# Kernel tuning notes

Measured on AMD Instinct MI355X. Metric: run time of the kernel, lower is better.

Reference implementation:

```python
import jax, jax.numpy as jnp
import numpy as np

NEG = -1e30  # log-space 'zero' (safe substitute for -inf)
EPS = 1e-7   # keras.backend.epsilon(), used by ctc_batch_cost


def _ctc_forward(logp, z, allow2):
    """CTC negative log-likelihood via the forward DP in log space.
    logp:   [B, T, C] log-probabilities
    z:      [B, S] extended label sequence (blanks interleaved), S = 2L+1
    allow2: [B, S] bool, whether the skip transition (s-2 -> s) is legal
    Returns [B, 1] loss (matches keras ctc_batch_cost output shape).
    """
    B, T, C = logp.shape
    S = z.shape[1]
    # Gather per-timestep log-probs of extended labels: [B, T, S] -> [T, B, S]
    b_idx = jnp.arange(B)[:, None, None]
    t_idx = jnp.arange(T)[None, :, None]
    lp_z = jnp.transpose(logp[b_idx, t_idx, z[:, None, :]], (1, 0, 2))

    s_idx = jnp.arange(S)[None, :]
    alpha0 = jnp.where(s_idx < 2, lp_z[0], NEG)  # paths may start at blank or first label

    def step(alpha, lp_t):
        a1 = jnp.concatenate([jnp.full((B, 1), NEG, alpha.dtype), alpha[:, :-1]], axis=1)
        a2 = jnp.concatenate([jnp.full((B, 2), NEG, alpha.dtype), alpha[:, :-2]], axis=1)
        a2 = jnp.where(allow2, a2, NEG)
        m = jnp.maximum(alpha, jnp.maximum(a1, a2))
        lse = m + jnp.log(jnp.exp(alpha - m) + jnp.exp(a1 - m) + jnp.exp(a2 - m))
        return lp_t + lse, None

    alphaT, _ = jax.lax.scan(step, alpha0, lp_z[1:])
    # Paths end at last blank (S-1) or last label (S-2)
    last, last2 = alphaT[:, -1], alphaT[:, -2]
    m = jnp.maximum(last, last2)
    ll = m + jnp.log(jnp.exp(last - m) + jnp.exp(last2 - m))
    return -ll[:, None]


def setup_inputs() -> dict:
    key = jax.random.key(0)
    k1, k2 = jax.random.split(key)
    B, T, C, L = 32, 2048, 256, 256
    # ctc_batch_cost expects post-softmax probabilities
    y_pred = jax.nn.softmax(jax.random.normal(k1, (B, T, C), jnp.float32), axis=-1)
    y_true = jax.random.randint(k2, (B, L), 0, C - 1)  # blank = C-1 excluded from labels
    return {"y_true": y_true, "y_pred": y_pred}


def reference(y_true, y_pred):
    B, T, C = y_pred.shape
    blank = C - 1
    L = y_true.shape[1]
    S = 2 * L + 1
    labels = y_true.astype(jnp.int32)
    # Extended label sequence: blank, l0, blank, l1, ..., blank
    z = jnp.full((B, S), blank, jnp.int32).at[:, 1::2].set(labels)
    z_m2 = jnp.concatenate([jnp.full((B, 2), -1, jnp.int32), z[:, :-2]], axis=1)
    allow2 = (z != blank) & (z != z_m2)
    logp = jnp.log(y_pred + EPS)
    return _ctc_forward(logp, z, allow2)
```

## Files before the change

### kernel.cpp

```cpp
#include <hip/hip_runtime.h>

#define TT   2048
#define CC   256
#define LL   256
#define SS   513
#define TM   1023
#define EPSF (1e-7f)
#define LN2F (0.69314718055994531f)
#define DPTH 8
#define RBTH 64
#define NCH  127
#define EMINI (-2000000000)
#define GSTR 260

#if __has_builtin(__builtin_amdgcn_frexp_expf)
#define FREXP_EXP __builtin_amdgcn_frexp_expf
#else
static __device__ __forceinline__ int FREXP_EXP(float x){ int e; return (frexpf(x,&e), e); }
#endif
#if __has_builtin(__builtin_amdgcn_ldexpf)
#define LDEXP __builtin_amdgcn_ldexpf
#else
#define LDEXP ldexpf
#endif

__launch_bounds__(256, 4)
__global__ void ctc_gather_kernel(const int* __restrict__ y_true,
                                  const float* __restrict__ y_pred,
                                  float* __restrict__ gat)
{
    const int b   = blockIdx.x;
    const int i   = threadIdx.x;
    const int col = y_true[b * LL + i];
    const float* rp = y_pred + (size_t)b * TT * CC;
    float*       gp = gat    + (size_t)b * TT * GSTR;
    const int tch = TT / gridDim.y;
    const int t0  = blockIdx.y * tch;
    #pragma unroll 4
    for (int t = t0; t < t0 + tch; ++t) {
        gp[(size_t)t * GSTR + i] = rp[(size_t)t * CC + col] + EPSF;
        if (i < 4)
            gp[(size_t)t * GSTR + 256 + i] = rp[(size_t)t * CC + (CC - 1)] + EPSF;
    }
}

template<int NSTEP>
__device__ __forceinline__ void fwd_group(float (&f)[9], int &e, bool &mm,
        const float (&kk)[8], int lane,
        float4 o0, float4 o1, float4 o2, float4 o3,
        float4 q0, float4 q1, float4 q2, float4 q3,
        float b0, float b1, float b2, float b3)
{
    float h[8];
    #pragma unroll
    for (int j = 0; j < 8; ++j) h[j] = __shfl_up(f[j], 1);
    int he = __shfl_up(e, 1);
    if (lane == 0) {
        he = e;
        #pragma unroll
        for (int j = 0; j < 8; ++j) h[j] = 0.0f;
    }
    const int E  = mm ? (e > he ? e : he) : he;
    const int dh = he - E, dn = e - E;
    float g[17];
    #pragma unroll
    for (int j = 0; j < 8; ++j) g[j] = LDEXP(h[j], dh);
    #pragma unroll
    for (int j = 0; j < 9; ++j) g[8 + j] = LDEXP(f[j], dn);
    e = E;

#define FSW(Q, O, B, LO) do {                                                 \
        const float pv[8] = {Q.x,Q.y,Q.z,Q.w,O.x,O.y,O.z,O.w};                \
        _Pragma("unroll")                                                     \
        for (int i = 16; i >= (LO); --i) {                                    \
            if (i & 1) g[i] = (g[i] + g[i-1] + g[i-2]*kk[(i-1)>>1])           \
                              * pv[(i-1)>>1];                                 \
            else       g[i] = (g[i] + g[i-1]) * (B);                          \
        }                                                                     \
    } while (0)

    if (NSTEP == 4) {
        FSW(q0,o0,b0,2); FSW(q1,o1,b1,4); FSW(q2,o2,b2,6); FSW(q3,o3,b3,8);
    } else {
        FSW(q0,o0,b0,4); FSW(q1,o1,b1,6); FSW(q2,o2,b2,8);
    }
#undef FSW

    #pragma unroll
    for (int j = 0; j < 9; ++j) f[j] = g[8 + j];
    float mx = f[0];
    #pragma unroll
    for (int j = 1; j < 9; ++j) mx = fmaxf(mx, f[j]);
    const int em = FREXP_EXP(mx);
    #pragma unroll
    for (int j = 0; j < 9; ++j) f[j] = LDEXP(f[j], -em);
    e += em;
    mm = (mx > 0.0f);
}

template<int NSTEP>
__device__ __forceinline__ void bwd_group(float (&f)[9], int &e, bool &mm,
        const float (&kk)[8], int lane,
        float4 o0, float4 o1, float4 o2, float4 o3,
        float4 q0, float4 q1, float4 q2, float4 q3,
        float b0, float b1, float b2, float b3)
{
    float h[8];
    #pragma unroll
    for (int j = 0; j < 8; ++j) h[j] = __shfl_down(f[j + 1], 1);
    int he = __shfl_down(e, 1);
    if (lane == 63) {
        he = e;
        #pragma unroll
        for (int j = 0; j < 8; ++j) h[j] = 0.0f;
    }
    const int E  = mm ? (e > he ? e : he) : he;
    const int dh = he - E, dn = e - E;
    float g[17];
    #pragma unroll
    for (int j = 0; j < 9; ++j) g[j] = LDEXP(f[j], dn);
    #pragma unroll
    for (int j = 0; j < 8; ++j) g[9 + j] = LDEXP(h[j], dh);
    e = E;

#define BSW(O, Q, B, HI) do {                                                 \
        const float pv[8] = {O.x,O.y,O.z,O.w,Q.x,Q.y,Q.z,Q.w};                \
        _Pragma("unroll")                                                     \
        for (int i = 0; i <= (HI); ++i) {                                     \
            if (i & 1) g[i] = (g[i] + g[i+1] + g[i+2]*kk[(i-1)>>1])           \
                              * pv[(i-1)>>1];                                 \
            else       g[i] = (g[i] + g[i+1]) * (B);                          \
        }                                                                     \
    } while (0)

    if (NSTEP == 4) {
        BSW(o0,q0,b0,14); BSW(o1,q1,b1,12); BSW(o2,q2,b2,10); BSW(o3,q3,b3,8);
    } else {
        BSW(o0,q0,b0,12); BSW(o1,q1,b1,10); BSW(o2,q2,b2,8);
    }
#undef BSW

    #pragma unroll
    for (int j = 0; j < 9; ++j) f[j] = g[j];
    float mx = f[0];
    #pragma unroll
    for (int j = 1; j < 9; ++j) mx = fmaxf(mx, f[j]);
    const int em = FREXP_EXP(mx);
    #pragma unroll
    for (int j = 0; j < 9; ++j) f[j] = LDEXP(f[j], -em);
    e += em;
    mm = (mx > 0.0f);
}

__launch_bounds__(128, 1)
__global__ void ctc_grp_kernel(const int* __restrict__ y_true,
                               const float* __restrict__ y_pred,
                               const float* __restrict__ gat,
                               float* __restrict__ out)
{
    __shared__ float cw[SS];
    __shared__ int   ew[64];

    const int tid   = threadIdx.x;
    const int w     = tid >> 6;
    const int lane  = tid & 63;
    const int b     = blockIdx.x;
    const int blank = CC - 1;

    const int*   lab  = y_true + b * LL;
    const float* base = y_pred + (size_t)b * TT * CC;
    const float* gLb  = gat    + (size_t)b * TT * GSTR;

    float kk[8];
    if (w == 0) {
        #pragma unroll
        for (int j = 0; j < 8; ++j) {
            const int li  = 4 * lane - 4 + j;
            const int lic = li < 0 ? 0 : li;
            const int z   = lab[lic];
            const int zm  = (li >= 1) ? lab[li - 1] : -1;
            kk[j] = (li >= 0 && z != zm) ? 1.0f : 0.0f;
        }
    } else {
        #pragma unroll
        for (int j = 0; j < 8; ++j) {
            const int li  = 4 * lane + j;
            const int lic = li > 255 ? 255 : li;
            const int z   = lab[lic];
            kk[j] = (li <= 254 && lab[li + 1] != z) ? 1.0f : 0.0f;
        }
    }

    float f[9];
    #pragma unroll
    for (int j = 0; j < 9; ++j) f[j] = 0.0f;
    int  e = 0;
    bool mm;

    if (w == 0) {
        if (lane == 0) {
            f[0] = base[blank]  + EPSF;
            f[1] = base[lab[0]] + EPSF;
        }
        mm = (lane == 0);
    } else {
        if (lane == 63) {
            const float* rT = base + (size_t)(TT - 1) * CC;
            f[7] = rT[lab[255]] + EPSF;
            f[8] = rT[blank]    + EPSF;
        }
        mm = (lane == 63);
    }

    const int oofs = 4 * lane;
    const int qofs = (w == 0) ? (4 * lane - 4 < 0 ? 0 : 4 * lane - 4)
                              : (4 * lane + 4);
    const int bofs = 256 + (lane & 3);
    const int dstp = (w == 0) ? GSTR : -GSTR;

    float4 s0o[4], s0q[4]; float s0b[4];

#define LOADG(SO, SQ, SB, ROWP) do {                                          \
        const float* _rp = (ROWP);                                            \
        _Pragma("unroll")                                                     \
        for (int k = 0; k < 4; ++k) {                                         \
            SO[k] = *(const float4*)(_rp + oofs);                             \
            SQ[k] = *(const float4*)(_rp + qofs);                             \
            SB[k] = _rp[bofs];                                                \
            _rp += dstp;                                                      \
        } } while (0)

    const float* grow = (w == 0) ? (gLb + (size_t)1 * GSTR)
                                 : (gLb + (size_t)2046 * GSTR);
    LOADG(s0o, s0q, s0b, grow); grow += 4 * dstp;

    for (int c = 0; c < 255; ++c) {
        const float4 a0 = s0o[0], a1 = s0o[1], a2 = s0o[2], a3 = s0o[3];
        const float4 p0 = s0q[0], p1 = s0q[1], p2 = s0q[2], p3 = s0q[3];
        const float  c0 = s0b[0], c1 = s0b[1], c2 = s0b[2], c3 = s0b[3];
        LOADG(s0o, s0q, s0b, grow); grow += 4 * dstp;
        __builtin_amdgcn_sched_barrier(0);
        if (w == 0) fwd_group<4>(f, e, mm, kk, lane,
                        a0,a1,a2,a3, p0,p1,p2,p3, c0,c1,c2,c3);
        else        bwd_group<4>(f, e, mm, kk, lane,
                        a0,a1,a2,a3, p0,p1,p2,p3, c0,c1,c2,c3);
    }
    {
        const float4 a0 = s0o[0], a1 = s0o[1], a2 = s0o[2], a3 = s0o[3];
        const float4 p0 = s0q[0], p1 = s0q[1], p2 = s0q[2], p3 = s0q[3];
        const float  c0 = s0b[0], c1 = s0b[1], c2 = s0b[2], c3 = s0b[3];
        if (w == 0) fwd_group<3>(f, e, mm, kk, lane,
                        a0,a1,a2,a3, p0,p1,p2,p3, c0,c1,c2,c3);
        else        bwd_group<3>(f, e, mm, kk, lane,
                        a0,a1,a2,a3, p0,p1,p2,p3, c0,c1,c2,c3);
    }
#undef LOADG

    if (w == 1) {
        float d1 = __shfl_down(f[1], 1);
        int   de = __shfl_down(e, 1);
        if (lane == 63) { d1 = 0.0f; de = e; }
        int dlt = de - e;
        if (dlt >= RBTH) {
            #pragma unroll
            for (int j = 0; j < 9; ++j) f[j] = LDEXP(f[j], -dlt);
            e = de; dlt = 0;
        }
        const float bf = LDEXP(d1, dlt);
        float cb[9];
        cb[0] = f[0] + f[1];
        cb[1] = f[1] + f[2] + f[3] * kk[0];
        cb[2] = f[2] + f[3];
        cb[3] = f[3] + f[4] + f[5] * kk[1];
        cb[4] = f[4] + f[5];
        cb[5] = f[5] + f[6] + f[7] * kk[2];
        cb[6] = f[6] + f[7];
        cb[7] = f[7] + f[8] + bf   * kk[3];
        cb[8] = f[8] + bf;
        #pragma unroll
        for (int j = 0; j < 8; ++j) cw[8 * lane + j] = cb[j];
        if (lane == 63) cw[512] = cb[8];
        ew[lane] = e;
    }

    __syncthreads();

    if (w == 0) {
        float part = 0.0f;
        #pragma unroll
        for (int j = 0; j < 8; ++j) part += f[j] * cw[8 * lane + j];
        if (lane == 63) part += f[8] * cw[512];
        int   ep = (part > 0.0f) ? (e + ew[lane]) : EMINI;
        float m  = part;
        #pragma unroll
        for (int d = 1; d < 64; d <<= 1) {
            const float mo = __shfl_xor(m, d);
            const int   eo = __shfl_xor(ep, d);
            const int   E  = ep > eo ? ep : eo;
            m  = LDEXP(m, ep - E) + LDEXP(mo, eo - E);
            ep = E;
        }
        if (lane == 0)
            out[b] = -LN2F * ((float)ep + __builtin_amdgcn_logf(m));
    }
}

__launch_bounds__(128, 1)
__global__ void ctc_fb_kernel(const int* __restrict__ y_true,
                              const float* __restrict__ y_pred,
                              float* __restrict__ out)
{
    __shared__ float cw[SS];
    __shared__ int   ew[64];

    const int tid   = threadIdx.x;
    const int w     = tid >> 6;
    const int lane  = tid & 63;
    const int b     = blockIdx.x;
    const int blank = CC - 1;

    const int*   lab  = y_true + b * LL;
    const float* base = y_pred + (size_t)b * TT * CC;

    int   col[4];
    float kup[4], kdn[4];
    #pragma unroll
    for (int i = 0; i < 4; ++i) {
        const int li = 4 * lane + i;
        const int z  = lab[li];
        col[i] = z;
        const int zm = (li >= 1) ? lab[li - 1] : -1;
        kup[i] = (z != zm) ? 1.0f : 0.0f;
        kdn[i] = (li <= 254 && lab[li + 1] != z) ? 1.0f : 0.0f;
    }

    float f[9];
    #pragma unroll
    for (int j = 0; j < 9; ++j) f[j] = 0.0f;
    int  e = 0;
    bool lzero;

    if (w == 0) {
        if (lane == 0) { f[0] = base[blank] + EPSF; f[1] = base[col[0]] + EPSF; }
        lzero = (lane != 0);
    } else {
        if (lane == 63) {
            const float* rT = base + (size_t)(TT - 1) * CC;
            f[7] = rT[col[3]] + EPSF; f[8] = rT[blank] + EPSF;
        }
        lzero = (lane != 63);
    }

    float pfb[DPTH]; float pfl[DPTH][4];
    #pragma unroll
    for (int k = 0; k < DPTH; ++k) {
        const int r = (w == 0) ? (1 + k) : (TT - 2 - k);
        const float* rp = base + (size_t)r * CC;
        pfb[k] = rp[blank];
        #pragma unroll
        for (int i = 0; i < 4; ++i) pfl[k][i] = rp[col[i]];
    }

    auto renorm = [&]() {
        float m = fmaxf(fmaxf(fmaxf(f[0], f[1]), fmaxf(f[2], f[3])),
                        fmaxf(fmaxf(f[4], f[5]), fmaxf(f[6], fmaxf(f[7], f[8]))));
        const int em = FREXP_EXP(m);
        #pragma unroll
        for (int j = 0; j < 9; ++j) f[j] = LDEXP(f[j], -em);
        e += em;
    };
    auto fwd_step = [&](float pb, float p0, float p1, float p2, float p3) {
        float u7 = __shfl_up(f[7], 1);
        int   ue = __shfl_up(e, 1);
        if (lane == 0) { u7 = 0.0f; ue = e; }
        int dlt = ue - e;
        const bool rb = lzero || (dlt >= RBTH);
        if (__ballot(rb)) {
            const int sh = rb ? -dlt : 0;
            #pragma unroll
            for (int j = 0; j < 9; ++j) f[j] = LDEXP(f[j], sh);
            e = rb ? ue : e; dlt = rb ? 0 : dlt;
            lzero = lzero && (u7 == 0.0f);
        }
        const float bf = LDEXP(u7, dlt);
        const float n0 = (f[0] + bf) * pb;
        const float n1 = (f[1] + f[0] + bf   * kup[0]) * p0;
        const float n2 = (f[2] + f[1]) * pb;
        const float n3 = (f[3] + f[2] + f[1] * kup[1]) * p1;
        const float n4 = (f[4] + f[3]) * pb;
        const float n5 = (f[5] + f[4] + f[3] * kup[2]) * p2;
        const float n6 = (f[6] + f[5]) * pb;
        const float n7 = (f[7] + f[6] + f[5] * kup[3]) * p3;
        const float n8 = (f[8] + f[7]) * pb;
        f[0]=n0; f[1]=n1; f[2]=n2; f[3]=n3; f[4]=n4;
        f[5]=n5; f[6]=n6; f[7]=n7; f[8]=n8;
    };
    auto bwd_step = [&](float pb, float p0, float p1, float p2, float p3) {
        float d1 = __shfl_down(f[1], 1);
        int   de = __shfl_down(e, 1);
        if (lane == 63) { d1 = 0.0f; de = e; }
        int dlt = de - e;
        const bool rb = lzero || (dlt >= RBTH);
        if (__ballot(rb)) {
            const int sh = rb ? -dlt : 0;
            #pragma unroll
            for (int j = 0; j < 9; ++j) f[j] = LDEXP(f[j], sh);
            e = rb ? de : e; dlt = rb ? 0 : dlt;
            lzero = lzero && (d1 == 0.0f);
        }
        const float bf = LDEXP(d1, dlt);
        const float n0 = (f[0] + f[1]) * pb;
        const float n1 = (f[1] + f[2] + f[3] * kdn[0]) * p0;
        const float n2 = (f[2] + f[3]) * pb;
        const float n3 = (f[3] + f[4] + f[5] * kdn[1]) * p1;
        const float n4 = (f[4] + f[5]) * pb;
        const float n5 = (f[5] + f[6] + f[7] * kdn[2]) * p2;
        const float n6 = (f[6] + f[7]) * pb;
        const float n7 = (f[7] + f[8] + bf   * kdn[3]) * p3;
        const float n8 = (f[8] + bf) * pb;
        f[0]=n0; f[1]=n1; f[2]=n2; f[3]=n3; f[4]=n4;
        f[5]=n5; f[6]=n6; f[7]=n7; f[8]=n8;
    };

    if (w == 0) {
        for (int c = 0; c < NCH; ++c) {
            #pragma unroll
            for (int k = 0; k < DPTH; ++k) {
                const float pb = pfb[k] + EPSF;
                const float p0 = pfl[k][0] + EPSF, p1 = pfl[k][1] + EPSF;
                const float p2 = pfl[k][2] + EPSF, p3 = pfl[k][3] + EPSF;
                int tp = 1 + c * DPTH + k + DPTH; if (tp > TM) tp = TM;
                const float* rp = base + (size_t)tp * CC;
                pfb[k] = rp[blank];
                #pragma unroll
                for (int i = 0; i < 4; ++i) pfl[k][i] = rp[col[i]];
                fwd_step(pb, p0, p1, p2, p3);
                if (k == 3 || k == 7) renorm();
            }
        }
        #pragma unroll
        for (int k = 0; k < 7; ++k) {
            fwd_step(pfb[k] + EPSF, pfl[k][0] + EPSF, pfl[k][1] + EPSF,
                     pfl[k][2] + EPSF, pfl[k][3] + EPSF);
            if (k == 3) renorm();
        }
    } else {
        for (int c = 0; c < NCH; ++c) {
            #pragma unroll
            for (int k = 0; k < DPTH; ++k) {
                const float pb = pfb[k] + EPSF;
                const float p0 = pfl[k][0] + EPSF, p1 = pfl[k][1] + EPSF;
                const float p2 = pfl[k][2] + EPSF, p3 = pfl[k][3] + EPSF;
                int tp = (TT - 2) - (c * DPTH + k) - DPTH; if (tp < TM + 1) tp = TM + 1;
                const float* rp = base + (size_t)tp * CC;
                pfb[k] = rp[blank];
                #pragma unroll
                for (int i = 0; i < 4; ++i) pfl[k][i] = rp[col[i]];
                bwd_step(pb, p0, p1, p2, p3);
                if (k == 3 || k == 7) renorm();
            }
        }
        #pragma unroll
        for (int k = 0; k < 7; ++k) {
            bwd_step(pfb[k] + EPSF, pfl[k][0] + EPSF, pfl[k][1] + EPSF,
                     pfl[k][2] + EPSF, pfl[k][3] + EPSF);
            if (k == 3) renorm();
        }

        float d1 = __shfl_down(f[1], 1);
        int   de = __shfl_down(e, 1);
        if (lane == 63) { d1 = 0.0f; de = e; }
        int dlt = de - e;
        if (dlt >= RBTH) {
            #pragma unroll
            for (int j = 0; j < 9; ++j) f[j] = LDEXP(f[j], -dlt);
            e = de; dlt = 0;
        }
        const float bf = LDEXP(d1, dlt);
        float cb[9];
        cb[0] = f[0] + f[1];
        cb[1] = f[1] + f[2] + f[3] * kdn[0];
        cb[2] = f[2] + f[3];
        cb[3] = f[3] + f[4] + f[5] * kdn[1];
        cb[4] = f[4] + f[5];
        cb[5] = f[5] + f[6] + f[7] * kdn[2];
        cb[6] = f[6] + f[7];
        cb[7] = f[7] + f[8] + bf   * kdn[3];
        cb[8] = f[8] + bf;
        #pragma unroll
        for (int j = 0; j < 8; ++j) cw[8 * lane + j] = cb[j];
        if (lane == 63) cw[512] = cb[8];
        ew[lane] = e;
    }

    __syncthreads();

    if (w == 0) {
        float part = 0.0f;
        #pragma unroll
        for (int j = 0; j < 8; ++j) part += f[j] * cw[8 * lane + j];
        if (lane == 63) part += f[8] * cw[512];
        int   ep = (part > 0.0f) ? (e + ew[lane]) : EMINI;
        float m  = part;
        #pragma unroll
        for (int d = 1; d < 64; d <<= 1) {
            const float mo = __shfl_xor(m, d);
            const int   eo = __shfl_xor(ep, d);
            const int   E  = ep > eo ? ep : eo;
            m  = LDEXP(m, ep - E) + LDEXP(mo, eo - E);
            ep = E;
        }
        if (lane == 0)
            out[b] = -LN2F * ((float)ep + __builtin_amdgcn_logf(m));
    }
}

extern "C" void kernel_launch(void* const* d_in, const int* in_sizes, int n_in,
                              void* d_out, int out_size, void* d_ws, size_t ws_size,
                              hipStream_t stream)
{
    const int*   y_true = (const int*)d_in[0];
    const float* y_pred = (const float*)d_in[1];
    float*       out    = (float*)d_out;
    const int B = in_sizes[0] / LL;

    const size_t need = (size_t)B * TT * GSTR * sizeof(float);
    if (ws_size >= need) {
        float* gat = (float*)d_ws;
        ctc_gather_kernel<<<dim3(B, 32), 256, 0, stream>>>(y_true, y_pred, gat);
        ctc_grp_kernel<<<B, 128, 0, stream>>>(y_true, y_pred, gat, out);
    } else {
        ctc_fb_kernel<<<B, 128, 0, stream>>>(y_true, y_pred, out);
    }
}
```

Baseline: 176.8 us.

## Split each CTC direction across two wavefronts with LDS halo exchange

The forward and backward recurrences are each spread over two wavefronts instead of one, so every lane holds 4 states instead of 8 and the per-step serial work per lane roughly halves. Neighbouring wavefronts exchange boundary states through double-buffered shared memory, with a block-wide barrier at every 4-timestep group. The final combine reduces across two partial sums. The per-group barrier and shared-memory round trip add latency to every step, which may offset the shorter dependency chain.

```diff
diff --git a/kernel.cpp b/kernel.cpp
--- a/kernel.cpp
+++ b/kernel.cpp
@@ -44,264 +44,317 @@
     }
 }
 
-template<int NSTEP>
-__device__ __forceinline__ void fwd_group(float (&f)[9], int &e, bool &mm,
-        const float (&kk)[8], int lane,
-        float4 o0, float4 o1, float4 o2, float4 o3,
-        float4 q0, float4 q1, float4 q2, float4 q3,
-        float b0, float b1, float b2, float b3)
+template<int NS>
+__device__ __forceinline__ void fwd_swp(float (&g)[13], const float (&kk)[6],
+        const float2 (&A)[4], const float2 (&B)[4], const float2 (&C)[4],
+        const float (&bl)[4])
 {
-    float h[8];
-    #pragma unroll
-    for (int j = 0; j < 8; ++j) h[j] = __shfl_up(f[j], 1);
-    int he = __shfl_up(e, 1);
-    if (lane == 0) {
-        he = e;
-        #pragma unroll
-        for (int j = 0; j < 8; ++j) h[j] = 0.0f;
-    }
-    const int E  = mm ? (e > he ? e : he) : he;
-    const int dh = he - E, dn = e - E;
-    float g[17];
-    #pragma unroll
-    for (int j = 0; j < 8; ++j) g[j] = LDEXP(h[j], dh);
-    #pragma unroll
-    for (int j = 0; j < 9; ++j) g[8 + j] = LDEXP(f[j], dn);
-    e = E;
-
-#define FSW(Q, O, B, LO) do {                                                 \
-        const float pv[8] = {Q.x,Q.y,Q.z,Q.w,O.x,O.y,O.z,O.w};                \
+#define FS(K, LO) do {                                                        \
+        const float pv[6] = {A[K].x,A[K].y,B[K].x,B[K].y,C[K].x,C[K].y};      \
+        const float pb = bl[K];                                               \
         _Pragma("unroll")                                                     \
-        for (int i = 16; i >= (LO); --i) {                                    \
+        for (int i = 12; i >= (LO); --i) {                                    \
             if (i & 1) g[i] = (g[i] + g[i-1] + g[i-2]*kk[(i-1)>>1])           \
                               * pv[(i-1)>>1];                                 \
-            else       g[i] = (g[i] + g[i-1]) * (B);                          \
+            else       g[i] = (g[i] + g[i-1]) * pb;                           \
         }                                                                     \
     } while (0)
-
-    if (NSTEP == 4) {
-        FSW(q0,o0,b0,2); FSW(q1,o1,b1,4); FSW(q2,o2,b2,6); FSW(q3,o3,b3,8);
-    } else {
-        FSW(q0,o0,b0,4); FSW(q1,o1,b1,6); FSW(q2,o2,b2,8);
-    }
-#undef FSW
-
-    #pragma unroll
-    for (int j = 0; j < 9; ++j) f[j] = g[8 + j];
-    float mx = f[0];
-    #pragma unroll
-    for (int j = 1; j < 9; ++j) mx = fmaxf(mx, f[j]);
-    const int em = FREXP_EXP(mx);
-    #pragma unroll
-    for (int j = 0; j < 9; ++j) f[j] = LDEXP(f[j], -em);
-    e += em;
-    mm = (mx > 0.0f);
+    if (NS == 4) { FS(0,2); FS(1,4); FS(2,6); FS(3,8); }
+    else         { FS(0,4); FS(1,6); FS(2,8); }
+#undef FS
 }
 
-template<int NSTEP>
-__device__ __forceinline__ void bwd_group(float (&f)[9], int &e, bool &mm,
-        const float (&kk)[8], int lane,
-        float4 o0, float4 o1, float4 o2, float4 o3,
-        float4 q0, float4 q1, float4 q2, float4 q3,
-        float b0, float b1, float b2, float b3)
+template<int NS>
+__device__ __forceinline__ void bwd_swp(float (&g)[13], const float (&kk)[6],
+        const float2 (&A)[4], const float2 (&B)[4], const float2 (&C)[4],
+        const float (&bl)[4])
 {
-    float h[8];
-    #pragma unroll
-    for (int j = 0; j < 8; ++j) h[j] = __shfl_down(f[j + 1], 1);
-    int he = __shfl_down(e, 1);
-    if (lane == 63) {
-        he = e;
-        #pragma unroll
-        for (int j = 0; j < 8; ++j) h[j] = 0.0f;
-    }
-    const int E  = mm ? (e > he ? e : he) : he;
-    const int dh = he - E, dn = e - E;
-    float g[17];
-    #pragma unroll
-    for (int j = 0; j < 9; ++j) g[j] = LDEXP(f[j], dn);
-    #pragma unroll
-    for (int j = 0; j < 8; ++j) g[9 + j] = LDEXP(h[j], dh);
-    e = E;
-
-#define BSW(O, Q, B, HI) do {                                                 \
-        const float pv[8] = {O.x,O.y,O.z,O.w,Q.x,Q.y,Q.z,Q.w};                \
+#define BS(K, HI) do {                                                        \
+        const float pv[6] = {A[K].x,A[K].y,B[K].x,B[K].y,C[K].x,C[K].y};      \
+        const float pb = bl[K];                                               \
         _Pragma("unroll")                                                     \
         for (int i = 0; i <= (HI); ++i) {                                     \
             if (i & 1) g[i] = (g[i] + g[i+1] + g[i+2]*kk[(i-1)>>1])           \
                               * pv[(i-1)>>1];                                 \
-            else       g[i] = (g[i] + g[i+1]) * (B);                          \
+            else       g[i] = (g[i] + g[i+1]) * pb;                           \
         }                                                                     \
     } while (0)
-
-    if (NSTEP == 4) {
-        BSW(o0,q0,b0,14); BSW(o1,q1,b1,12); BSW(o2,q2,b2,10); BSW(o3,q3,b3,8);
-    } else {
-        BSW(o0,q0,b0,12); BSW(o1,q1,b1,10); BSW(o2,q2,b2,8);
-    }
-#undef BSW
-
-    #pragma unroll
-    for (int j = 0; j < 9; ++j) f[j] = g[j];
-    float mx = f[0];
-    #pragma unroll
-    for (int j = 1; j < 9; ++j) mx = fmaxf(mx, f[j]);
-    const int em = FREXP_EXP(mx);
-    #pragma unroll
-    for (int j = 0; j < 9; ++j) f[j] = LDEXP(f[j], -em);
-    e += em;
-    mm = (mx > 0.0f);
+    if (NS == 4) { BS(0,10); BS(1,8); BS(2,6); BS(3,4); }
+    else         { BS(0,8);  BS(1,6); BS(2,4); }
+#undef BS
 }
 
-__launch_bounds__(128, 1)
-__global__ void ctc_grp_kernel(const int* __restrict__ y_true,
-                               const float* __restrict__ y_pred,
-                               const float* __restrict__ gat,
-                               float* __restrict__ out)
+__launch_bounds__(256, 1)
+__global__ void ctc_ms_kernel(const int* __restrict__ y_true,
+                              const float* __restrict__ y_pred,
+                              const float* __restrict__ gat,
+                              float* __restrict__ out)
 {
     __shared__ float cw[SS];
-    __shared__ int   ew[64];
-
-    const int tid   = threadIdx.x;
-    const int w     = tid >> 6;
-    const int lane  = tid & 63;
-    const int b     = blockIdx.x;
+    __shared__ int   ew[128];
+    __shared__ float hF[2][2][2][4];
+    __shared__ int   hE[2][2][2];
+    __shared__ float jf1s_; __shared__ int je_s_;
+    __shared__ float pm[2]; __shared__ int pe[2];
+
+    const int tid  = threadIdx.x;
+    const int w    = tid >> 6;
+    const int lane = tid & 63;
+    const int dir  = (w >= 2) ? 1 : 0;
+    const int sub  = w & 1;
+    const int b    = blockIdx.x;
     const int blank = CC - 1;
 
     const int*   lab  = y_true + b * LL;
     const float* base = y_pred + (size_t)b * TT * CC;
     const float* gLb  = gat    + (size_t)b * TT * GSTR;
 
-    float kk[8];
-    if (w == 0) {
-        #pragma unroll
-        for (int j = 0; j < 8; ++j) {
-            const int li  = 4 * lane - 4 + j;
-            const int lic = li < 0 ? 0 : li;
-            const int z   = lab[lic];
-            const int zm  = (li >= 1) ? lab[li - 1] : -1;
-            kk[j] = (li >= 0 && z != zm) ? 1.0f : 0.0f;
-        }
-    } else {
-        #pragma unroll
-        for (int j = 0; j < 8; ++j) {
-            const int li  = 4 * lane + j;
-            const int lic = li > 255 ? 255 : li;
-            const int z   = lab[lic];
-            kk[j] = (li <= 254 && lab[li + 1] != z) ? 1.0f : 0.0f;
-        }
-    }
-
-    float f[9];
+    const int L0 = 2 * (64 * sub + lane);
+
+    float kk[6];
     #pragma unroll
-    for (int j = 0; j < 9; ++j) f[j] = 0.0f;
+    for (int m = 0; m < 6; ++m) {
+        if (dir == 0) {
+            const int l  = L0 - 4 + m;
+            const int lc = l < 0 ? 0 : l;
+            const int lp = (l - 1) < 0 ? 0 : (l - 1);
+            kk[m] = (l >= 0 && (l == 0 || lab[lc] != lab[lp])) ? 1.0f : 0.0f;
+        } else {
+            const int l  = L0 + m;
+            const int lc = l > 255 ? 255 : l;
+            const int l1 = (l + 1) > 255 ? 255 : (l + 1);
+            kk[m] = ((l + 1) <= 255 && lab[l1] != lab[lc]) ? 1.0f : 0.0f;
+        }
+    }
+
+    float f[5];
+    #pragma unroll
+    for (int j = 0; j < 5; ++j) f[j] = 0.0f;
     int  e = 0;
     bool mm;
-
-    if (w == 0) {
-        if (lane == 0) {
+    if (dir == 0) {
+        if (w == 0 && lane == 0) {
             f[0] = base[blank]  + EPSF;
             f[1] = base[lab[0]] + EPSF;
         }
-        mm = (lane == 0);
+        mm = (w == 0 && lane == 0);
     } else {
-        if (lane == 63) {
+        if (w == 3 && lane == 63) {
             const float* rT = base + (size_t)(TT - 1) * CC;
-            f[7] = rT[lab[255]] + EPSF;
-            f[8] = rT[blank]    + EPSF;
-        }
-        mm = (lane == 63);
-    }
-
-    const int oofs = 4 * lane;
-    const int qofs = (w == 0) ? (4 * lane - 4 < 0 ? 0 : 4 * lane - 4)
-                              : (4 * lane + 4);
+            f[3] = rT[lab[255]] + EPSF;
+            f[4] = rT[blank]    + EPSF;
+        }
+        mm = (w == 3 && lane == 63);
+    }
+
+    const int o0 = dir ? L0 : (L0 - 4 < 0 ? 0 : L0 - 4);
+    const int o1 = dir ? (L0 + 2 > 254 ? 254 : L0 + 2) : (L0 - 2 < 0 ? 0 : L0 - 2);
+    const int o2 = dir ? (L0 + 4 > 254 ? 254 : L0 + 4) : L0;
     const int bofs = 256 + (lane & 3);
-    const int dstp = (w == 0) ? GSTR : -GSTR;
-
-    float4 s0o[4], s0q[4]; float s0b[4];
-
-#define LOADG(SO, SQ, SB, ROWP) do {                                          \
-        const float* _rp = (ROWP);                                            \
+    const int dstp = dir ? -GSTR : GSTR;
+
+    float2 sA[4], sB[4], sC[4]; float sbl[4];
+    const float* grow = dir ? (gLb + (size_t)2046 * GSTR)
+                            : (gLb + (size_t)1 * GSTR);
+
+#define LOADG do { const float* _rp = grow;                                   \
         _Pragma("unroll")                                                     \
         for (int k = 0; k < 4; ++k) {                                         \
-            SO[k] = *(const float4*)(_rp + oofs);                             \
-            SQ[k] = *(const float4*)(_rp + qofs);                             \
-            SB[k] = _rp[bofs];                                                \
+            sA[k] = *(const float2*)(_rp + o0);                               \
+            sB[k] = *(const float2*)(_rp + o1);                               \
+            sC[k] = *(const float2*)(_rp + o2);                               \
+            sbl[k] = _rp[bofs];                                               \
             _rp += dstp;                                                      \
-        } } while (0)
-
-    const float* grow = (w == 0) ? (gLb + (size_t)1 * GSTR)
-                                 : (gLb + (size_t)2046 * GSTR);
-    LOADG(s0o, s0q, s0b, grow); grow += 4 * dstp;
-
-    for (int c = 0; c < 255; ++c) {
-        const float4 a0 = s0o[0], a1 = s0o[1], a2 = s0o[2], a3 = s0o[3];
-        const float4 p0 = s0q[0], p1 = s0q[1], p2 = s0q[2], p3 = s0q[3];
-        const float  c0 = s0b[0], c1 = s0b[1], c2 = s0b[2], c3 = s0b[3];
-        LOADG(s0o, s0q, s0b, grow); grow += 4 * dstp;
+        }                                                                     \
+        grow += 4 * dstp; } while (0)
+
+    LOADG;
+
+    if (w == 0 && lane >= 62) {
+        #pragma unroll
+        for (int j = 0; j < 4; ++j) hF[0][0][lane - 62][j] = f[j];
+        hE[0][0][lane - 62] = e;
+    }
+    if (w == 3 && lane <= 1) {
+        #pragma unroll
+        for (int j = 0; j < 4; ++j) hF[0][1][lane][j] = f[j + 1];
+        hE[0][1][lane] = e;
+    }
+
+    for (int c = 0; c < 256; ++c) {
+        float2 A[4], B[4], C[4]; float bl[4];
+        #pragma unroll
+        for (int k = 0; k < 4; ++k) { A[k]=sA[k]; B[k]=sB[k]; C[k]=sC[k]; bl[k]=sbl[k]; }
+        if (c < 255) { LOADG; }
         __builtin_amdgcn_sched_barrier(0);
-        if (w == 0) fwd_group<4>(f, e, mm, kk, lane,
-                        a0,a1,a2,a3, p0,p1,p2,p3, c0,c1,c2,c3);
-        else        bwd_group<4>(f, e, mm, kk, lane,
-                        a0,a1,a2,a3, p0,p1,p2,p3, c0,c1,c2,c3);
-    }
-    {
-        const float4 a0 = s0o[0], a1 = s0o[1], a2 = s0o[2], a3 = s0o[3];
-        const float4 p0 = s0q[0], p1 = s0q[1], p2 = s0q[2], p3 = s0q[3];
-        const float  c0 = s0b[0], c1 = s0b[1], c2 = s0b[2], c3 = s0b[3];
-        if (w == 0) fwd_group<3>(f, e, mm, kk, lane,
-                        a0,a1,a2,a3, p0,p1,p2,p3, c0,c1,c2,c3);
-        else        bwd_group<3>(f, e, mm, kk, lane,
-                        a0,a1,a2,a3, p0,p1,p2,p3, c0,c1,c2,c3);
+        __syncthreads();
+        const int cbuf = c & 1, nbuf = (c + 1) & 1;
+
+        float h1[4], h2[4]; int e1, e2;
+        if (dir == 0) {
+            #pragma unroll
+            for (int j = 0; j < 4; ++j) { h1[j] = __shfl_up(f[j], 1);
+                                          h2[j] = __shfl_up(f[j], 2); }
+            e1 = __shfl_up(e, 1); e2 = __shfl_up(e, 2);
+            if (sub == 0) {
+                if (lane == 0) {
+                    #pragma unroll
+                    for (int j = 0; j < 4; ++j) { h1[j] = 0.0f; h2[j] = 0.0f; }
+                    e1 = e; e2 = e;
+                } else if (lane == 1) {
+                    #pragma unroll
+                    for (int j = 0; j < 4; ++j) h2[j] = 0.0f;
+                    e2 = e1;
+                }
+            } else {
+                if (lane == 0) {
+                    #pragma unroll
+                    for (int j = 0; j < 4; ++j) { h1[j] = hF[cbuf][0][1][j];
+                                                  h2[j] = hF[cbuf][0][0][j]; }
+                    e1 = hE[cbuf][0][1]; e2 = hE[cbuf][0][0];
+                } else if (lane == 1) {
+                    #pragma unroll
+                    for (int j = 0; j < 4; ++j) h2[j] = hF[cbuf][0][1][j];
+                    e2 = hE[cbuf][0][1];
+                }
+            }
+        } else {
+            #pragma unroll
+            for (int j = 0; j < 4; ++j) { h1[j] = __shfl_down(f[j + 1], 1);
+                                          h2[j] = __shfl_down(f[j + 1], 2); }
+            e1 = __shfl_down(e, 1); e2 = __shfl_down(e, 2);
+            if (sub == 1) {
+                if (lane == 63) {
+                    #pragma unroll
+                    for (int j = 0; j < 4; ++j) { h1[j] = 0.0f; h2[j] = 0.0f; }
+                    e1 = e; e2 = e;
+                } else if (lane == 62) {
+                    #pragma unroll
+                    for (int j = 0; j < 4; ++j) h2[j] = 0.0f;
+                    e2 = e1;
+                }
+            } else {
+                if (lane == 63) {
+                    #pragma unroll
+                    for (int j = 0; j < 4; ++j) { h1[j] = hF[cbuf][1][0][j];
+                                                  h2[j] = hF[cbuf][1][1][j]; }
+                    e1 = hE[cbuf][1][0]; e2 = hE[cbuf][1][1];
+                } else if (lane == 62) {
+                    #pragma unroll
+                    for (int j = 0; j < 4; ++j) h2[j] = hF[cbuf][1][0][j];
+                    e2 = hE[cbuf][1][0];
+                }
+            }
+        }
+
+        const int Eh = e1 > e2 ? e1 : e2;
+        const int E  = mm ? (e > Eh ? e : Eh) : Eh;
+        const int da = e1 - E, db = e2 - E, dn = e - E;
+        float g[13];
+        if (dir == 0) {
+            #pragma unroll
+            for (int j = 0; j < 4; ++j) g[j]     = LDEXP(h2[j], db);
+            #pragma unroll
+            for (int j = 0; j < 4; ++j) g[4 + j] = LDEXP(h1[j], da);
+            #pragma unroll
+            for (int j = 0; j < 5; ++j) g[8 + j] = LDEXP(f[j], dn);
+        } else {
+            #pragma unroll
+            for (int j = 0; j < 5; ++j) g[j]     = LDEXP(f[j], dn);
+            #pragma unroll
+            for (int j = 0; j < 4; ++j) g[5 + j] = LDEXP(h1[j], da);
+            #pragma unroll
+            for (int j = 0; j < 4; ++j) g[9 + j] = LDEXP(h2[j], db);
+        }
+        e = E;
+
+        if (c < 255) {
+            if (dir == 0) fwd_swp<4>(g, kk, A, B, C, bl);
+            else          bwd_swp<4>(g, kk, A, B, C, bl);
+        } else {
+            if (dir == 0) fwd_swp<3>(g, kk, A, B, C, bl);
+            else          bwd_swp<3>(g, kk, A, B, C, bl);
+        }
+
+        if (dir == 0) {
+            #pragma unroll
+            for (int j = 0; j < 5; ++j) f[j] = g[8 + j];
+        } else {
+            #pragma unroll
+            for (int j = 0; j < 5; ++j) f[j] = g[j];
+        }
+        float mx = f[0];
+        #pragma unroll
+        for (int j = 1; j < 5; ++j) mx = fmaxf(mx, f[j]);
+        const int em = FREXP_EXP(mx);
+        #pragma unroll
+        for (int j = 0; j < 5; ++j) f[j] = LDEXP(f[j], -em);
+        e += em;
+        mm = (mx > 0.0f);
+
+        if (c < 255) {
+            if (w == 0 && lane >= 62) {
+                #pragma unroll
+                for (int j = 0; j < 4; ++j) hF[nbuf][0][lane - 62][j] = f[j];
+                hE[nbuf][0][lane - 62] = e;
+            }
+            if (w == 3 && lane <= 1) {
+                #pragma unroll
+                for (int j = 0; j < 4; ++j) hF[nbuf][1][lane][j] = f[j + 1];
+                hE[nbuf][1][lane] = e;
+            }
+        }
     }
 #undef LOADG
 
-    if (w == 1) {
+    if (w == 3 && lane == 0) { jf1s_ = f[1]; je_s_ = e; }
+    __syncthreads();
+
+    if (dir == 1) {
         float d1 = __shfl_down(f[1], 1);
         int   de = __shfl_down(e, 1);
-        if (lane == 63) { d1 = 0.0f; de = e; }
+        if (sub == 0 && lane == 63) { d1 = jf1s_; de = je_s_; }
+        if (sub == 1 && lane == 63) { d1 = 0.0f; de = e; }
         int dlt = de - e;
         if (dlt >= RBTH) {
             #pragma unroll
-            for (int j = 0; j < 9; ++j) f[j] = LDEXP(f[j], -dlt);
+            for (int j = 0; j < 5; ++j) f[j] = LDEXP(f[j], -dlt);
             e = de; dlt = 0;
         }
         const float bf = LDEXP(d1, dlt);
-        float cb[9];
-        cb[0] = f[0] + f[1];
-        cb[1] = f[1] + f[2] + f[3] * kk[0];
-        cb[2] = f[2] + f[3];
-        cb[3] = f[3] + f[4] + f[5] * kk[1];
-        cb[4] = f[4] + f[5];
-        cb[5] = f[5] + f[6] + f[7] * kk[2];
-        cb[6] = f[6] + f[7];
-        cb[7] = f[7] + f[8] + bf   * kk[3];
-        cb[8] = f[8] + bf;
-        #pragma unroll
-        for (int j = 0; j < 8; ++j) cw[8 * lane + j] = cb[j];
-        if (lane == 63) cw[512] = cb[8];
-        ew[lane] = e;
-    }
-
+        const int c0 = 4 * (64 * sub + lane);
+        cw[c0 + 0] = f[0] + f[1];
+        cw[c0 + 1] = f[1] + f[2] + f[3] * kk[0];
+        cw[c0 + 2] = f[2] + f[3];
+        cw[c0 + 3] = f[3] + f[4] + bf * kk[1];
+        if (sub == 1 && lane == 63) cw[512] = f[4];
+        ew[sub * 64 + lane] = e;
+    }
     __syncthreads();
 
-    if (w == 0) {
-        float part = 0.0f;
-        #pragma unroll
-        for (int j = 0; j < 8; ++j) part += f[j] * cw[8 * lane + j];
-        if (lane == 63) part += f[8] * cw[512];
-        int   ep = (part > 0.0f) ? (e + ew[lane]) : EMINI;
+    if (dir == 0) {
+        const int c0 = 4 * (64 * sub + lane);
+        float part = f[0]*cw[c0] + f[1]*cw[c0+1] + f[2]*cw[c0+2] + f[3]*cw[c0+3];
+        if (sub == 1 && lane == 63) part += f[4] * cw[512];
+        int   ep = (part > 0.0f) ? (e + ew[sub * 64 + lane]) : EMINI;
         float m  = part;
         #pragma unroll
         for (int d = 1; d < 64; d <<= 1) {
             const float mo = __shfl_xor(m, d);
             const int   eo = __shfl_xor(ep, d);
-            const int   E  = ep > eo ? ep : eo;
-            m  = LDEXP(m, ep - E) + LDEXP(mo, eo - E);
-            ep = E;
-        }
-        if (lane == 0)
-            out[b] = -LN2F * ((float)ep + __builtin_amdgcn_logf(m));
+            const int   E2 = ep > eo ? ep : eo;
+            m  = LDEXP(m, ep - E2) + LDEXP(mo, eo - E2);
+            ep = E2;
+        }
+        if (lane == 0) { pm[sub] = m; pe[sub] = ep; }
+    }
+    __syncthreads();
+    if (tid == 0) {
+        const float m0 = pm[0], m1 = pm[1];
+        const int   p0 = pe[0], p1 = pe[1];
+        const int   E2 = p0 > p1 ? p0 : p1;
+        const float m  = LDEXP(m0, p0 - E2) + LDEXP(m1, p1 - E2);
+        out[b] = -LN2F * ((float)E2 + __builtin_amdgcn_logf(m));
     }
 }
 
@@ -528,7 +581,7 @@
     if (ws_size >= need) {
         float* gat = (float*)d_ws;
         ctc_gather_kernel<<<dim3(B, 32), 256, 0, stream>>>(y_true, y_pred, gat);
-        ctc_grp_kernel<<<B, 128, 0, stream>>>(y_true, y_pred, gat, out);
+        ctc_ms_kernel<<<B, 256, 0, stream>>>(y_true, y_pred, gat, out);
     } else {
         ctc_fb_kernel<<<B, 128, 0, stream>>>(y_true, y_pred, out);
     }
```

New measurement: 275.2 us. +55.7%, slower.
